# Kernel optimization log

Hardware: AMD Instinct MI355X
Metric: run time of the kernel (lower is better)

The kernel has to match this reference:

```python
import jax, jax.numpy as jnp
import numpy as np

COMMITMENT_COST = 0.25


def setup_inputs() -> dict:
    key = jax.random.key(0)
    k1, k2 = jax.random.split(key)
    N, K, D = 131072, 1024, 64
    inputs = jax.random.normal(k1, (N, D), dtype=jnp.float32)
    # torch init: uniform(-1/K, 1/K); use randn scaled similarly-small for a generic table
    embedding = jax.random.uniform(k2, (K, D), dtype=jnp.float32,
                                   minval=-1.0 / K, maxval=1.0 / K)
    return {"inputs": inputs, "embedding": embedding}


def reference(inputs, embedding):
    distances = (jnp.sum(inputs ** 2, axis=1, keepdims=True)
                 + jnp.sum(embedding ** 2, axis=1)
                 - 2.0 * inputs @ embedding.T)
    encoding_indices = jnp.argmin(distances, axis=1)            # [N]
    # direct gather (same math as one-hot @ embedding)
    quantized = embedding[encoding_indices]                     # [N, D]

    diff2 = jnp.mean((quantized - inputs) ** 2)
    # e_latent_loss == q_latent_loss numerically in fwd
    loss = diff2 + COMMITMENT_COST * diff2

    # straight-through output (forward value == quantized)
    quantized_st = inputs + jax.lax.stop_gradient(quantized - inputs)

    # avg_probs via histogram instead of materializing [N, K] one-hot
    N, K = inputs.shape[0], embedding.shape[0]
    counts = jnp.zeros((K,), dtype=jnp.float32).at[encoding_indices].add(1.0)
    avg_probs = counts / N
    perplexity = jnp.exp(-jnp.sum(avg_probs * jnp.log(avg_probs + 1e-10)))

    return quantized_st, loss, encoding_indices.reshape(N, 1), perplexity
```

## Files before the change

### kernel.cpp

```cpp
#include <hip/hip_runtime.h>
#include <hip/hip_bf16.h>

#define D 64
#define MARGIN 8e-5f
#define RB 8

typedef __attribute__((ext_vector_type(8))) short bf16x8;
typedef __attribute__((ext_vector_type(4))) float f32x4;
typedef __attribute__((ext_vector_type(4))) unsigned uint4v;


__device__ __forceinline__ float np_pairwise_sumsq64(const float* a) {
    float r[8];
#pragma unroll
    for (int j = 0; j < 8; ++j) r[j] = __fmul_rn(a[j], a[j]);
#pragma unroll
    for (int i = 8; i < 64; i += 8)
#pragma unroll
        for (int j = 0; j < 8; ++j)
            r[j] = __fadd_rn(r[j], __fmul_rn(a[i + j], a[i + j]));
    return __fadd_rn(
        __fadd_rn(__fadd_rn(r[0], r[1]), __fadd_rn(r[2], r[3])),
        __fadd_rn(__fadd_rn(r[4], r[5]), __fadd_rn(r[6], r[7])));
}

#define CVT8(F0, F1, H, L)                                                    \
    do {                                                                      \
        float _f[8] = {F0.x, F0.y, F0.z, F0.w, F1.x, F1.y, F1.z, F1.w};       \
        _Pragma("unroll") for (int _i = 0; _i < 8; ++_i) {                    \
            unsigned _u = __float_as_uint(_f[_i]);                            \
            unsigned _hb = (_u + 0x7fffu + ((_u >> 16) & 1u)) >> 16;          \
            float _hf = __uint_as_float(_hb << 16);                           \
            float _r = _f[_i] - _hf;                                          \
            unsigned _u2 = __float_as_uint(_r);                               \
            unsigned _lb = (_u2 + 0x7fffu + ((_u2 >> 16) & 1u)) >> 16;        \
            H[_i] = (short)_hb;                                               \
            L[_i] = (short)_lb;                                               \
        }                                                                     \
    } while (0)

__global__ __launch_bounds__(256) void vq_prep_all(
    const float* __restrict__ emb, int K,
    float* __restrict__ eenp, float* __restrict__ neh,
    unsigned short* __restrict__ ehs, float* __restrict__ eT,
    unsigned* __restrict__ counts, unsigned* __restrict__ done,
    unsigned* __restrict__ nunc) {
    int b = blockIdx.x;
    if (b < 64) {
        int t = b * 256 + threadIdx.x;
        int tile = t >> 8, r = t & 255, s = r >> 6, l = r & 63;
        int sub = l & 15, grp = l >> 4;
        int k = tile * 16 + sub;
        int d0 = ((s & 1) << 5) + (grp << 3);
        const float* e = emb + (size_t)k * D + d0;
        float4 f0 = *(const float4*)e;
        float4 f1 = *(const float4*)(e + 4);
        bf16x8 h, lo;
        CVT8(f0, f1, h, lo);
        *(bf16x8*)(ehs + (size_t)t * 8) = (s >> 1) ? lo : h;
    } else if (b < 68) {
        int k = (b - 64) * 256 + threadIdx.x;
        float s = np_pairwise_sumsq64(emb + (size_t)k * D);
        eenp[k] = s;
        neh[k] = -0.5f * s;
    } else if (b < 324) {
        int t = (b - 68) * 256 + threadIdx.x;
        int d = t / K, k = t - d * K;
        eT[t] = emb[(size_t)k * D + d];
    } else {
#pragma unroll
        for (int i = 0; i < 4; ++i) {
            int c = threadIdx.x + 256 * i;
            if (c < K) counts[c] = 0u;
        }
        if (threadIdx.x == 0) { *done = 0u; *nunc = 0u; }
    }
}

__global__ __launch_bounds__(512) void vq_main(
    const float* __restrict__ x, const unsigned short* __restrict__ ehs,
    const float* __restrict__ neh, const float* __restrict__ emb,
    int N, int K,
    float* __restrict__ outq, float* __restrict__ outidx,
    double* __restrict__ lossA,
    unsigned* __restrict__ nunc, unsigned* __restrict__ list) {
    const int tid = threadIdx.x;
    const int lane = tid & 63;
    const int wid = tid >> 6;
    const int half = wid >> 2;
    const int wq = wid & 3;
    const int rows0 = blockIdx.x * 256;
    const int row0 = rows0 + wq * 64;
    const int sub = lane & 15, grp = lane >> 4;
    const int g4 = grp << 2;
    const int k0 = half * (K >> 1);
    const int NT = (K >> 1) >> 4;
    const int t0 = k0 >> 4;

    __shared__ __align__(16) unsigned short lds[2][2][2048];
    __shared__ float sm1[2][256], sm2[2][256], sxx[256];
    __shared__ int sdec[256];
    __shared__ double ls[4];

    bf16x8 xh[4][2], xl[4][2];
    float xq[4];
#pragma unroll
    for (int rt = 0; rt < 4; ++rt) {
        xq[rt] = 0.f;
        const float* xrow = x + (((size_t)(row0 + (rt << 4) + sub)) << 6) + (grp << 3);
#pragma unroll
        for (int s = 0; s < 2; ++s) {
            float4 f0 = *(const float4*)(xrow + (s << 5));
            float4 f1 = *(const float4*)(xrow + (s << 5) + 4);
            xq[rt] = fmaf(f0.x, f0.x, xq[rt]); xq[rt] = fmaf(f0.y, f0.y, xq[rt]);
            xq[rt] = fmaf(f0.z, f0.z, xq[rt]); xq[rt] = fmaf(f0.w, f0.w, xq[rt]);
            xq[rt] = fmaf(f1.x, f1.x, xq[rt]); xq[rt] = fmaf(f1.y, f1.y, xq[rt]);
            xq[rt] = fmaf(f1.z, f1.z, xq[rt]); xq[rt] = fmaf(f1.w, f1.w, xq[rt]);
            CVT8(f0, f1, xh[rt][s], xl[rt][s]);
        }
    }
#pragma unroll
    for (int rt = 0; rt < 4; ++rt) {
        xq[rt] += __shfl_xor(xq[rt], 16);
        xq[rt] += __shfl_xor(xq[rt], 32);
    }

    float m1[4], m2[4];
#pragma unroll
    for (int rt = 0; rt < 4; ++rt) { m1[rt] = -3e38f; m2[rt] = -3e38f; }

    const unsigned short* sbase = ehs + ((size_t)t0 << 11);
    const int slot = (wq << 9) + (lane << 3);

    uint4v tmp = *(const uint4v*)(sbase + slot);
    *(uint4v*)&lds[half][0][slot] = tmp;
    __syncthreads();

    for (int t = 0; t < NT; ++t) {
        const int cur = t & 1;
        if (t + 1 < NT)
            tmp = *(const uint4v*)(sbase + ((size_t)(t + 1) << 11) + slot);

        f32x4 cb = *(const f32x4*)(neh + k0 + (t << 4) + g4);
        const bf16x8* L = (const bf16x8*)&lds[half][cur][0];
        bf16x8 a0 = L[lane];
        bf16x8 a1 = L[64 + lane];
        bf16x8 a2 = L[128 + lane];
        bf16x8 a3 = L[192 + lane];

        f32x4 acc[4];
#pragma unroll
        for (int rt = 0; rt < 4; ++rt)
            acc[rt] = __builtin_amdgcn_mfma_f32_16x16x32_bf16(a0, xh[rt][0], cb, 0, 0, 0);
#pragma unroll
        for (int rt = 0; rt < 4; ++rt)
            acc[rt] = __builtin_amdgcn_mfma_f32_16x16x32_bf16(a2, xh[rt][0], acc[rt], 0, 0, 0);
#pragma unroll
        for (int rt = 0; rt < 4; ++rt)
            acc[rt] = __builtin_amdgcn_mfma_f32_16x16x32_bf16(a0, xl[rt][0], acc[rt], 0, 0, 0);
#pragma unroll
        for (int rt = 0; rt < 4; ++rt)
            acc[rt] = __builtin_amdgcn_mfma_f32_16x16x32_bf16(a1, xh[rt][1], acc[rt], 0, 0, 0);
#pragma unroll
        for (int rt = 0; rt < 4; ++rt)
            acc[rt] = __builtin_amdgcn_mfma_f32_16x16x32_bf16(a3, xh[rt][1], acc[rt], 0, 0, 0);
#pragma unroll
        for (int rt = 0; rt < 4; ++rt)
            acc[rt] = __builtin_amdgcn_mfma_f32_16x16x32_bf16(a1, xl[rt][1], acc[rt], 0, 0, 0);

        const int baset = 511 - (t << 4) - g4;
#pragma unroll
        for (int rt = 0; rt < 4; ++rt) {
#pragma unroll
            for (int j = 0; j < 4; ++j) {
                unsigned pv = (__float_as_uint(acc[rt][j]) & 0xFFFFFE00u)
                              | (unsigned)(baset - j);
                float p = __uint_as_float(pv);
                m2[rt] = fminf(fmaxf(p, m2[rt]), m1[rt]);
                m1[rt] = fmaxf(p, m1[rt]);
            }
        }

        if (t + 1 < NT)
            *(uint4v*)&lds[half][cur ^ 1][slot] = tmp;
        __syncthreads();
    }

#pragma unroll
    for (int rt = 0; rt < 4; ++rt) {
#pragma unroll
        for (int off = 16; off <= 32; off <<= 1) {
            float om1 = __shfl_xor(m1[rt], off);
            float om2 = __shfl_xor(m2[rt], off);
            float lo = fminf(m1[rt], om1);
            m1[rt] = fmaxf(m1[rt], om1);
            m2[rt] = fmaxf(lo, fmaxf(m2[rt], om2));
        }
    }

    if (lane < 16) {
#pragma unroll
        for (int rt = 0; rt < 4; ++rt) {
            int lr = wq * 64 + (rt << 4) + lane;
            sm1[half][lr] = m1[rt];
            sm2[half][lr] = m2[rt];
            if (half == 0) sxx[lr] = xq[rt];
        }
    }
    __syncthreads();

    if (tid < 256) {
        const int lr = tid;
        const int r = rows0 + lr;
        float m1a = sm1[0][lr], m1b = sm1[1][lr];
        float m2a = sm2[0][lr], m2b = sm2[1][lr];
        bool take = m1b > m1a;
        float gm1 = fmaxf(m1a, m1b);
        float gm2 = fmaxf(fminf(m1a, m1b), fmaxf(m2a, m2b));
        int loc = 511 - (int)(__float_as_uint(gm1) & 511u);
        int k = (take ? (K >> 1) : 0) + loc;
        bool amb = 2.0f * (gm1 - gm2) < MARGIN;
        unsigned long long mask = __ballot(amb);
        int cnt = __popcll(mask);
        unsigned base = 0;
        if (lane == 0 && cnt) base = atomicAdd(nunc, (unsigned)cnt);
        base = __shfl(base, 0);
        int dec = k;
        double lpart = 0.0;
        if (amb) {
            int rank = __popcll(mask & ((1ull << lane) - 1ull));
            list[base + rank] = (unsigned)r;
            dec = -1;
        } else {
            outidx[r] = (float)dec;
            float gm1v = __uint_as_float(__float_as_uint(gm1) & 0xFFFFFE00u);
            lpart = (double)(sxx[lr] - 2.0f * gm1v);
        }
        sdec[lr] = dec;
#pragma unroll
        for (int off = 32; off; off >>= 1) lpart += __shfl_down(lpart, off);
        if (lane == 0) ls[wid] = lpart;
    }
    __syncthreads();
    if (tid == 0)
        lossA[blockIdx.x] = ls[0] + ls[1] + ls[2] + ls[3];

    const int chunk = tid & 15, rl = tid >> 4;
#pragma unroll
    for (int p = 0; p < 8; ++p) {
        int lr = p * 32 + rl;
        int dp = sdec[lr];
        if (dp >= 0) {
            float4 ev = *(const float4*)(emb + (size_t)dp * D + chunk * 4);
            *(float4*)(outq + (size_t)(rows0 + lr) * D + chunk * 4) = ev;
        }
    }
}

__global__ __launch_bounds__(256) void vq_resolve(
    const float* __restrict__ x, const float* __restrict__ emb,
    const float* __restrict__ eT, const float* __restrict__ eenp,
    int N, int K,
    float* __restrict__ outq, float* __restrict__ outidx,
    double* __restrict__ lossR,
    const unsigned* __restrict__ nunc, const unsigned* __restrict__ list) {
    const unsigned n = *nunc;
    const int tid = threadIdx.x;
    const int w = tid >> 6, l = tid & 63;
    const f32x4* eT4 = (const f32x4*)eT;
    __shared__ float sxr[RB][64];
    __shared__ float sxx[RB];
    __shared__ float swm[RB][4];
    __shared__ int swi[RB][4];
    __shared__ int sres[RB];
    double lacc = 0.0;

    for (unsigned base = blockIdx.x * RB; base < n; base += gridDim.x * RB) {
        const int nb = (int)(n - base < (unsigned)RB ? n - base : (unsigned)RB);
#pragma unroll
        for (int i = tid; i < RB * 64; i += 256) {
            int r = i >> 6, d = i & 63;
            if (r < nb) sxr[r][d] = x[(size_t)list[base + r] * D + d];
        }
        __syncthreads();
        if (tid < nb) sxx[tid] = np_pairwise_sumsq64(&sxr[tid][0]);
        __syncthreads();

        f32x4 dt[RB];
#pragma unroll
        for (int r = 0; r < RB; ++r) dt[r] = (f32x4){0.f, 0.f, 0.f, 0.f};
#pragma unroll 4
        for (int d = 0; d < D; ++d) {
            f32x4 ev = eT4[(size_t)d * 256 + tid];
#pragma unroll
            for (int r = 0; r < RB; ++r) {
                float xv = sxr[r][d];
                dt[r][0] = __fmaf_rn(xv, ev[0], dt[r][0]);
                dt[r][1] = __fmaf_rn(xv, ev[1], dt[r][1]);
                dt[r][2] = __fmaf_rn(xv, ev[2], dt[r][2]);
                dt[r][3] = __fmaf_rn(xv, ev[3], dt[r][3]);
            }
        }

#pragma unroll
        for (int r = 0; r < RB; ++r) {
            if (r >= nb) break;
            float xx = sxx[r];
            float bm = 1e30f;
            int bi = 0;
#pragma unroll
            for (int jj = 0; jj < 4; ++jj) {
                int k = (tid << 2) + jj;
                float dist = __fsub_rn(__fadd_rn(xx, eenp[k]),
                                       __fmul_rn(2.0f, dt[r][jj]));
                if (dist < bm) { bm = dist; bi = k; }
            }
#pragma unroll
            for (int off = 1; off < 64; off <<= 1) {
                float ov = __shfl_xor(bm, off);
                int oi = __shfl_xor(bi, off);
                if (ov < bm || (ov == bm && oi < bi)) { bm = ov; bi = oi; }
            }
            if (l == 0) { swm[r][w] = bm; swi[r][w] = bi; }
        }
        __syncthreads();
        if (tid < nb) {
            float fm = swm[tid][0];
            int fi = swi[tid][0];
#pragma unroll
            for (int ww = 1; ww < 4; ++ww) {
                float ov = swm[tid][ww];
                int oi = swi[tid][ww];
                if (ov < fm || (ov == fm && oi < fi)) { fm = ov; fi = oi; }
            }
            sres[tid] = fi;
            outidx[list[base + tid]] = (float)fi;
            lacc += (double)fm;
        }
        __syncthreads();
        for (int i = tid; i < RB * 64; i += 256) {
            int r = i >> 6, d = i & 63;
            if (r < nb)
                outq[(size_t)list[base + r] * D + d] =
                    emb[(size_t)sres[r] * D + d];
        }
        __syncthreads();
    }
#pragma unroll
    for (int off = 32; off; off >>= 1) lacc += __shfl_down(lacc, off);
    __shared__ double lsw;
    if (tid == 0) lsw = lacc;
    __syncthreads();
    if (tid == 0) lossR[blockIdx.x] = lsw;
}

__global__ __launch_bounds__(256) void vq_histperp(
    const float* __restrict__ outidx, int N, int K,
    unsigned* __restrict__ counts, unsigned* __restrict__ done,
    const double* __restrict__ lossA, int nA,
    const double* __restrict__ lossR, int nR,
    float* __restrict__ out_loss, float* __restrict__ out_perp) {
    __shared__ unsigned h[1024];
    __shared__ unsigned rank_s;
#pragma unroll
    for (int i = 0; i < 4; ++i) h[threadIdx.x + 256 * i] = 0;
    __syncthreads();
    int per = N / gridDim.x;
    int base = blockIdx.x * per;
    for (int i = threadIdx.x; i < per; i += 256) {
        int k = (int)outidx[base + i];
        atomicAdd(&h[k], 1u);
    }
    __syncthreads();
#pragma unroll
    for (int i = 0; i < 4; ++i) {
        int b = threadIdx.x + 256 * i;
        unsigned v = h[b];
        if (b < K && v) atomicAdd(counts + b, v);
    }
    __threadfence();
    if (threadIdx.x == 0) rank_s = atomicAdd(done, 1u);
    __syncthreads();
    if (rank_s == gridDim.x - 1) {
        double part = 0.0;
        for (int k = threadIdx.x; k < K; k += 256) {
            unsigned c = atomicAdd(counts + k, 0u);
            double p = (double)c / (double)N;
            part += p * log(p + 1e-10);
        }
        double lsum = 0.0;
        for (int i = threadIdx.x; i < nA; i += 256) lsum += lossA[i];
        for (int i = threadIdx.x; i < nR; i += 256) lsum += lossR[i];
#pragma unroll
        for (int off = 32; off; off >>= 1) {
            part += __shfl_down(part, off);
            lsum += __shfl_down(lsum, off);
        }
        __shared__ double ls[4], ls2[4];
        if ((threadIdx.x & 63) == 0) {
            ls[threadIdx.x >> 6] = part;
            ls2[threadIdx.x >> 6] = lsum;
        }
        __syncthreads();
        if (threadIdx.x == 0) {
            double s = ls[0] + ls[1] + ls[2] + ls[3];
            double L = ls2[0] + ls2[1] + ls2[2] + ls2[3];
            *out_perp = (float)exp(-s);
            *out_loss = (float)(1.25 * (L / ((double)N * (double)D)));
        }
    }
}

extern "C" void kernel_launch(void* const* d_in, const int* in_sizes, int n_in,
                              void* d_out, int out_size, void* d_ws, size_t ws_size,
                              hipStream_t stream) {
    const float* x = (const float*)d_in[0];
    const float* emb = (const float*)d_in[1];
    int N = in_sizes[0] / D;
    int K = in_sizes[1] / D;

    float* outq = (float*)d_out;
    float* out_loss = outq + (size_t)N * D;
    float* outidx = out_loss + 1;
    float* out_perp = outidx + N;

    char* ws = (char*)d_ws;
    unsigned* counts = (unsigned*)ws;
    unsigned* done = (unsigned*)(ws + (size_t)K * 4);
    unsigned* nunc = (unsigned*)(ws + (size_t)K * 4 + 4);
    size_t off = (size_t)K * 4 + 16;
    float* neh = (float*)(ws + off);            off += (size_t)K * 4;
    float* eenp = (float*)(ws + off);           off += (size_t)K * 4;
    unsigned short* ehs = (unsigned short*)(ws + off);  off += (size_t)K * 256;
    float* eT = (float*)(ws + off);              off += (size_t)K * D * 4;
    unsigned* list = (unsigned*)(ws + off);      off += (size_t)N * 4;
    int nA = N / 256, nR = 128;
    double* lossA = (double*)(ws + off);         off += (size_t)nA * 8;
    double* lossR = (double*)(ws + off);         off += (size_t)nR * 8;

    vq_prep_all<<<325, 256, 0, stream>>>(emb, K, eenp, neh, ehs, eT,
                                         counts, done, nunc);
    vq_main<<<N / 256, 512, 0, stream>>>(x, ehs, neh, emb, N, K,
                                         outq, outidx, lossA, nunc, list);
    vq_resolve<<<128, 256, 0, stream>>>(x, emb, eT, eenp, N, K,
                                        outq, outidx, lossR, nunc, list);
    vq_histperp<<<16, 256, 0, stream>>>(outidx, N, K, counts, done,
                                        lossA, nA, lossR, nR,
                                        out_loss, out_perp);
}
```

Before: 165.0 us.

## Split codebook halves across separate blocks with last-arriver global merge

```diff
diff --git a/kernel.cpp b/kernel.cpp
--- a/kernel.cpp
+++ b/kernel.cpp
@@ -40,11 +40,11 @@
     } while (0)
 
 __global__ __launch_bounds__(256) void vq_prep_all(
-    const float* __restrict__ emb, int K,
+    const float* __restrict__ emb, int K, int N,
     float* __restrict__ eenp, float* __restrict__ neh,
     unsigned short* __restrict__ ehs, float* __restrict__ eT,
     unsigned* __restrict__ counts, unsigned* __restrict__ done,
-    unsigned* __restrict__ nunc) {
+    unsigned* __restrict__ nunc, unsigned* __restrict__ gdone) {
     int b = blockIdx.x;
     if (b < 64) {
         int t = b * 256 + threadIdx.x;
@@ -73,33 +73,37 @@
             int c = threadIdx.x + 256 * i;
             if (c < K) counts[c] = 0u;
         }
+        int ng = N / 256;
+        for (int i = threadIdx.x; i < ng; i += 256) gdone[i] = 0u;
         if (threadIdx.x == 0) { *done = 0u; *nunc = 0u; }
     }
 }
 
-__global__ __launch_bounds__(512) void vq_main(
+__global__ __launch_bounds__(256) void vq_main(
     const float* __restrict__ x, const unsigned short* __restrict__ ehs,
     const float* __restrict__ neh, const float* __restrict__ emb,
     int N, int K,
+    float* __restrict__ m1p, float* __restrict__ m2p, float* __restrict__ xxp,
+    unsigned* __restrict__ gdone,
     float* __restrict__ outq, float* __restrict__ outidx,
     double* __restrict__ lossA,
     unsigned* __restrict__ nunc, unsigned* __restrict__ list) {
     const int tid = threadIdx.x;
     const int lane = tid & 63;
     const int wid = tid >> 6;
-    const int half = wid >> 2;
-    const int wq = wid & 3;
-    const int rows0 = blockIdx.x * 256;
-    const int row0 = rows0 + wq * 64;
+    const int kslice = blockIdx.x & 1;
+    const int rowblk = blockIdx.x >> 1;
+    const int rows0 = rowblk * 256;
+    const int row0 = rows0 + wid * 64;
     const int sub = lane & 15, grp = lane >> 4;
     const int g4 = grp << 2;
-    const int k0 = half * (K >> 1);
+    const int k0 = kslice * (K >> 1);
     const int NT = (K >> 1) >> 4;
     const int t0 = k0 >> 4;
 
-    __shared__ __align__(16) unsigned short lds[2][2][2048];
-    __shared__ float sm1[2][256], sm2[2][256], sxx[256];
+    __shared__ __align__(16) unsigned short lds[2][2048];
     __shared__ int sdec[256];
+    __shared__ int select;
     __shared__ double ls[4];
 
     bf16x8 xh[4][2], xl[4][2];
@@ -130,10 +134,10 @@
     for (int rt = 0; rt < 4; ++rt) { m1[rt] = -3e38f; m2[rt] = -3e38f; }
 
     const unsigned short* sbase = ehs + ((size_t)t0 << 11);
-    const int slot = (wq << 9) + (lane << 3);
+    const int slot = (wid << 9) + (lane << 3);
 
     uint4v tmp = *(const uint4v*)(sbase + slot);
-    *(uint4v*)&lds[half][0][slot] = tmp;
+    *(uint4v*)&lds[0][slot] = tmp;
     __syncthreads();
 
     for (int t = 0; t < NT; ++t) {
@@ -142,7 +146,7 @@
             tmp = *(const uint4v*)(sbase + ((size_t)(t + 1) << 11) + slot);
 
         f32x4 cb = *(const f32x4*)(neh + k0 + (t << 4) + g4);
-        const bf16x8* L = (const bf16x8*)&lds[half][cur][0];
+        const bf16x8* L = (const bf16x8*)&lds[cur][0];
         bf16x8 a0 = L[lane];
         bf16x8 a1 = L[64 + lane];
         bf16x8 a2 = L[128 + lane];
@@ -182,7 +186,7 @@
         }
 
         if (t + 1 < NT)
-            *(uint4v*)&lds[half][cur ^ 1][slot] = tmp;
+            *(uint4v*)&lds[cur ^ 1][slot] = tmp;
         __syncthreads();
     }
 
@@ -201,19 +205,26 @@
     if (lane < 16) {
 #pragma unroll
         for (int rt = 0; rt < 4; ++rt) {
-            int lr = wq * 64 + (rt << 4) + lane;
-            sm1[half][lr] = m1[rt];
-            sm2[half][lr] = m2[rt];
-            if (half == 0) sxx[lr] = xq[rt];
-        }
-    }
-    __syncthreads();
-
-    if (tid < 256) {
-        const int lr = tid;
-        const int r = rows0 + lr;
-        float m1a = sm1[0][lr], m1b = sm1[1][lr];
-        float m2a = sm2[0][lr], m2b = sm2[1][lr];
+            size_t idx = (size_t)kslice * N + row0 + (rt << 4) + lane;
+            m1p[idx] = m1[rt];
+            m2p[idx] = m2[rt];
+            if (kslice == 0) xxp[row0 + (rt << 4) + lane] = xq[rt];
+        }
+    }
+
+    __threadfence();
+    __syncthreads();
+    if (tid == 0) select = (int)atomicAdd(gdone + rowblk, 1u);
+    __syncthreads();
+    if (select == 0) return;
+
+    {
+        const int r = rows0 + tid;
+        float m1a = __uint_as_float(atomicAdd((unsigned*)&m1p[r], 0u));
+        float m1b = __uint_as_float(atomicAdd((unsigned*)&m1p[(size_t)N + r], 0u));
+        float m2a = __uint_as_float(atomicAdd((unsigned*)&m2p[r], 0u));
+        float m2b = __uint_as_float(atomicAdd((unsigned*)&m2p[(size_t)N + r], 0u));
+        float xxv = __uint_as_float(atomicAdd((unsigned*)&xxp[r], 0u));
         bool take = m1b > m1a;
         float gm1 = fmaxf(m1a, m1b);
         float gm2 = fmaxf(fminf(m1a, m1b), fmaxf(m2a, m2b));
@@ -234,21 +245,21 @@
         } else {
             outidx[r] = (float)dec;
             float gm1v = __uint_as_float(__float_as_uint(gm1) & 0xFFFFFE00u);
-            lpart = (double)(sxx[lr] - 2.0f * gm1v);
-        }
-        sdec[lr] = dec;
+            lpart = (double)(xxv - 2.0f * gm1v);
+        }
+        sdec[tid] = dec;
 #pragma unroll
         for (int off = 32; off; off >>= 1) lpart += __shfl_down(lpart, off);
         if (lane == 0) ls[wid] = lpart;
     }
     __syncthreads();
     if (tid == 0)
-        lossA[blockIdx.x] = ls[0] + ls[1] + ls[2] + ls[3];
+        lossA[rowblk] = ls[0] + ls[1] + ls[2] + ls[3];
 
     const int chunk = tid & 15, rl = tid >> 4;
 #pragma unroll
-    for (int p = 0; p < 8; ++p) {
-        int lr = p * 32 + rl;
+    for (int p = 0; p < 16; ++p) {
+        int lr = p * 16 + rl;
         int dp = sdec[lr];
         if (dp >= 0) {
             float4 ev = *(const float4*)(emb + (size_t)dp * D + chunk * 4);
@@ -434,17 +445,24 @@
     unsigned short* ehs = (unsigned short*)(ws + off);  off += (size_t)K * 256;
     float* eT = (float*)(ws + off);              off += (size_t)K * D * 4;
     unsigned* list = (unsigned*)(ws + off);      off += (size_t)N * 4;
-    int nA = N / 256, nR = 128;
-    double* lossA = (double*)(ws + off);         off += (size_t)nA * 8;
+    float* m1p = (float*)(ws + off);             off += (size_t)2 * N * 4;
+    float* m2p = (float*)(ws + off);             off += (size_t)2 * N * 4;
+    float* xxp = (float*)(ws + off);             off += (size_t)N * 4;
+    int nG = N / 256;
+    unsigned* gdone = (unsigned*)(ws + off);     off += (size_t)nG * 4;
+    double* lossA = (double*)(ws + off);         off += (size_t)nG * 8;
+    int nR = 128;
     double* lossR = (double*)(ws + off);         off += (size_t)nR * 8;
 
-    vq_prep_all<<<325, 256, 0, stream>>>(emb, K, eenp, neh, ehs, eT,
-                                         counts, done, nunc);
-    vq_main<<<N / 256, 512, 0, stream>>>(x, ehs, neh, emb, N, K,
-                                         outq, outidx, lossA, nunc, list);
+    vq_prep_all<<<325, 256, 0, stream>>>(emb, K, N, eenp, neh, ehs, eT,
+                                         counts, done, nunc, gdone);
+    vq_main<<<(N / 256) * 2, 256, 0, stream>>>(x, ehs, neh, emb, N, K,
+                                               m1p, m2p, xxp, gdone,
+                                               outq, outidx, lossA,
+                                               nunc, list);
     vq_resolve<<<128, 256, 0, stream>>>(x, emb, eT, eenp, N, K,
                                         outq, outidx, lossR, nunc, list);
     vq_histperp<<<16, 256, 0, stream>>>(outidx, N, K, counts, done,
-                                        lossA, nA, lossR, nR,
+                                        lossA, nG, lossR, nR,
                                         out_loss, out_perp);
 }
```

Result: slower. 249.0 us (+50.9%).
